# Optimization experiments

Measured on AMD Instinct MI355X. Metric: run time of the kernel, lower is better.

The kernel has to match this reference:

```python
import jax, jax.numpy as jnp
import numpy as np

SOM = (32, 32)   # som_dim; SOM[0]*SOM[1] == num_embeddings
LR = 0.05


def setup_inputs() -> dict:
    key = jax.random.key(0)
    k1, k2 = jax.random.split(key)
    B, K, D = 65536, 1024, 256
    x = jax.random.normal(k1, (B, D), dtype=jnp.float32)
    embeddings = jax.random.uniform(k2, (K, D), dtype=jnp.float32)  # torch.rand init
    return {"x": x, "embeddings": embeddings}


def reference(x, embeddings):
    K, D = embeddings.shape
    # pairwise squared distances: [B, K]
    dist = (jnp.sum(x * x, axis=1, keepdims=True)
            + jnp.sum(embeddings * embeddings, axis=1)
            - 2.0 * (x @ embeddings.T))
    n_min = jnp.argmin(dist, axis=1)          # [B]
    z_q = embeddings[n_min]                   # [B, D]

    # SOM grid coordinates and clamped neighbors
    n_x = n_min // SOM[1]
    n_y = n_min % SOM[1]
    x_up = jnp.where(n_x < SOM[0] - 1, n_x + 1, n_x)
    x_down = jnp.where(n_x > 0, n_x - 1, n_x)
    y_right = jnp.where(n_y < SOM[1] - 1, n_y + 1, n_y)
    y_left = jnp.where(n_y > 0, n_y - 1, n_y)
    idx_up = x_up * SOM[1] + n_y
    idx_down = x_down * SOM[1] + n_y
    idx_right = n_x * SOM[1] + y_right
    idx_left = n_x * SOM[1] + y_left

    # [B, 4, D] neighbor gather (order: up, down, left, right as in torch code)
    nbr_idx = jnp.stack([idx_up, idx_down, idx_left, idx_right], axis=1)
    z_q_neighbors = embeddings[nbr_idx]

    # SOM scatter update (torch does one-hot matmuls; segment_sum is the fused form)
    dw = x - z_q                              # [B, D]
    seg = lambda idx: jax.ops.segment_sum(dw, idx, num_segments=K)
    new_embeddings = jax.lax.stop_gradient(
        embeddings
        + LR * seg(n_min)
        + 0.5 * LR * (seg(idx_up) + seg(idx_down) + seg(idx_right) + seg(idx_left))
    )

    commit_loss = jnp.mean((x - z_q) ** 2)
    som_loss = jnp.mean((jax.lax.stop_gradient(x)[:, None, :] - z_q_neighbors) ** 2)
    return z_q, commit_loss, som_loss, new_embeddings
```

## Files before the change

### kernel.cpp

```cpp
#include <hip/hip_runtime.h>

#define B_ROWS 65536
#define DDIM   256
#define KEMB   1024
#define LRC    0.05f
#define BM 64
#define BN 128

typedef __attribute__((ext_vector_type(8))) _Float16 half8;
typedef __attribute__((ext_vector_type(4))) float f32x4;

#define SX_OFF    0u
#define CNT_OFF   1048576u
#define SUMS_OFF  1052672u
#define ESQ_OFF   1053312u
#define CUR_OFF   1057408u
#define NMIN_OFF  1061504u
#define ROWS_OFF  1585792u
#define EH_OFF    1847936u

static __device__ __forceinline__ unsigned short f2h(float f) {
  _Float16 h = (_Float16)f;
  return *(unsigned short*)&h;
}
static __device__ __forceinline__ float h2f(unsigned short u) {
  _Float16 h = *(_Float16*)&u;
  return (float)h;
}
static __device__ __forceinline__ void glds16(const void* g, void* l) {
  __builtin_amdgcn_global_load_lds(
      (const __attribute__((address_space(1))) unsigned int*)g,
      (__attribute__((address_space(3))) unsigned int*)l, 16, 0, 0);
}

__global__ __launch_bounds__(256) void convert_kernel(
    const float* __restrict__ E, unsigned short* __restrict__ Eh,
    float* __restrict__ esq) {
  size_t i = (size_t)blockIdx.x * 256 + threadIdx.x;
  size_t off = i * 8;
  const float4 v0 = *(const float4*)(E + off);
  const float4 v1 = *(const float4*)(E + off + 4);
  float f[8] = {v0.x, v0.y, v0.z, v0.w, v1.x, v1.y, v1.z, v1.w};
  unsigned short h[8];
  float part = 0.f;
#pragma unroll
  for (int j = 0; j < 8; ++j) {
    h[j] = f2h(f[j]);
    part += f[j] * f[j];
  }
  *(uint4*)(Eh + off) = *(const uint4*)h;
  float s = part;
  for (int o = 16; o > 0; o >>= 1) s += __shfl_down(s, o, 32);
  if ((threadIdx.x & 31) == 0) esq[i >> 5] = s;
}

__global__ __launch_bounds__(256, 2) void gemm_argmin_kernel(
    const float* __restrict__ X, const unsigned short* __restrict__ EhW,
    const float* __restrict__ esq, const float* __restrict__ Ef,
    int* __restrict__ nmin, int* __restrict__ counts, float* __restrict__ zq,
    double* __restrict__ sums) {
  __shared__ __align__(16) unsigned short sX[2][8][256][8];
  __shared__ __align__(16) unsigned short sE[2][512][8];

  const int tid  = threadIdx.x;
  const int lane = tid & 63, w = tid >> 6;
  const int lrow = lane & 15;
  const int qidx = lane >> 4;
  const int rowbase = (w >> 1) * 32;
  const int colb    = (w & 1) * 64;
  const int bm0 = (int)blockIdx.x * BM;

  int ec_row[2], ec_q8[2];
#pragma unroll
  for (int j = 0; j < 2; ++j) {
    const int c = j * 256 + tid;
    ec_row[j] = c >> 2;
    ec_q8[j]  = ((c & 3) ^ ((ec_row[j] >> 1) & 3)) * 8;
  }

#pragma unroll
  for (int j = 0; j < 2; ++j)
    glds16(EhW + (size_t)ec_row[j] * DDIM + ec_q8[j], (char*)&sE[0][j * 256 + tid][0]);

  {
    float part = 0.f;
#pragma unroll
    for (int it = 0; it < 8; ++it) {
      const int c   = it * 256 + tid;
      const int kcc = c >> 8;
      const int cc  = c & 255;
      const int row = cc >> 2;
      const int q   = (cc & 3) ^ ((row >> 1) & 3);
      const float* xp = X + (size_t)(bm0 + row) * DDIM + kcc * 32 + q * 8;
      const float4 a = *(const float4*)xp;
      const float4 b = *(const float4*)(xp + 4);
      float f[8] = {a.x, a.y, a.z, a.w, b.x, b.y, b.z, b.w};
      unsigned short hh[8], ll[8];
#pragma unroll
      for (int m = 0; m < 8; ++m) {
        hh[m] = f2h(f[m]);
        ll[m] = f2h(f[m] - h2f(hh[m]));
        part += f[m] * f[m];
      }
      *(uint4*)((char*)sX + (size_t)c * 16)          = *(const uint4*)hh;
      *(uint4*)((char*)sX + (size_t)(c + 2048) * 16) = *(const uint4*)ll;
    }
#pragma unroll
    for (int o = 32; o > 0; o >>= 1) part += __shfl_down(part, o);
    if (lane == 0)
      atomicAdd(&sums[8 + (((int)blockIdx.x * 4 + w) & 63)], (double)part);
  }

  float rbest[8];
  int   ridx[8];
#pragma unroll
  for (int i = 0; i < 8; ++i) { rbest[i] = 3.4e38f; ridx[i] = 0; }

  int ra[2], rb[4];
#pragma unroll
  for (int t = 0; t < 2; ++t) {
    const int m = rowbase + t * 16 + lrow;
    ra[t] = (m << 2) | (qidx ^ ((m >> 1) & 3));
  }
#pragma unroll
  for (int t = 0; t < 4; ++t) {
    const int n = colb + t * 16 + lrow;
    rb[t] = (n << 2) | (qidx ^ ((n >> 1) & 3));
  }

  __syncthreads();

  for (int nt = 0; nt < 8; ++nt) {
    f32x4 acc[2][4];
#pragma unroll
    for (int i = 0; i < 2; ++i)
#pragma unroll
      for (int j = 0; j < 4; ++j) acc[i][j] = (f32x4){0.f, 0.f, 0.f, 0.f};

#pragma unroll
    for (int kcc = 0; kcc < 8; ++kcc) {
      const int s   = nt * 8 + kcc;
      const int cur = s & 1;
      if (s < 63) {
        const int ns = s + 1;
        const int nnt = ns >> 3, nk = ns & 7;
#pragma unroll
        for (int j = 0; j < 2; ++j) {
          const int c = j * 256 + tid;
          glds16(EhW + (size_t)(nnt * BN + ec_row[j]) * DDIM + nk * 32 + ec_q8[j],
                 (char*)&sE[cur ^ 1][c][0]);
        }
      }
      half8 af0[2], af1[2], bfr[4];
#pragma unroll
      for (int t = 0; t < 2; ++t) {
        af0[t] = *(const half8*)&sX[0][kcc][ra[t]][0];
        af1[t] = *(const half8*)&sX[1][kcc][ra[t]][0];
      }
#pragma unroll
      for (int t = 0; t < 4; ++t) bfr[t] = *(const half8*)&sE[cur][rb[t]][0];
#pragma unroll
      for (int tr = 0; tr < 2; ++tr)
#pragma unroll
        for (int tc = 0; tc < 4; ++tc)
          acc[tr][tc] = __builtin_amdgcn_mfma_f32_16x16x32_f16(
              af0[tr], bfr[tc], acc[tr][tc], 0, 0, 0);
#pragma unroll
      for (int tr = 0; tr < 2; ++tr)
#pragma unroll
        for (int tc = 0; tc < 4; ++tc)
          acc[tr][tc] = __builtin_amdgcn_mfma_f32_16x16x32_f16(
              af1[tr], bfr[tc], acc[tr][tc], 0, 0, 0);
      __syncthreads();
    }
#pragma unroll
    for (int tc = 0; tc < 4; ++tc) {
      const int col = nt * BN + colb + tc * 16 + lrow;
      const float eq = esq[col];
#pragma unroll
      for (int tr = 0; tr < 2; ++tr)
#pragma unroll
        for (int rr = 0; rr < 4; ++rr) {
          float d = eq - 2.0f * acc[tr][tc][rr];
          const int slot = tr * 4 + rr;
          if (d < rbest[slot]) { rbest[slot] = d; ridx[slot] = col; }
        }
    }
  }

  float* cdd = (float*)&sE[0][0][0];
  int*   cdi = (int*)(cdd + 128);
  int*   snm = cdi + 128;
  int*   h   = (int*)&sX[0][0][0][0];

#pragma unroll
  for (int i = 0; i < 4; ++i) h[tid + i * 256] = 0;

#pragma unroll
  for (int slot = 0; slot < 8; ++slot) {
    float bd = rbest[slot];
    int   bi = ridx[slot];
#pragma unroll
    for (int off = 1; off < 16; off <<= 1) {
      float od = __shfl_xor(bd, off, 64);
      int   oi = __shfl_xor(bi, off, 64);
      if (od < bd || (od == bd && oi < bi)) { bd = od; bi = oi; }
    }
    if (lrow == 0) {
      const int row = rowbase + (slot >> 2) * 16 + (lane >> 4) * 4 + (slot & 3);
      cdd[(w & 1) * 64 + row] = bd;
      cdi[(w & 1) * 64 + row] = bi;
    }
  }
  __syncthreads();
  if (tid < BM) {
    float d0 = cdd[tid], d1 = cdd[64 + tid];
    int   i0 = cdi[tid], i1 = cdi[64 + tid];
    int bi = (d1 < d0 || (d1 == d0 && i1 < i0)) ? i1 : i0;
    nmin[bm0 + tid] = bi;
    snm[tid] = bi;
    atomicAdd(&h[bi], 1);
  }
  __syncthreads();
#pragma unroll
  for (int i = 0; i < 4; ++i) {
    int v = h[tid + i * 256];
    if (v) atomicAdd(&counts[tid + i * 256], v);
  }
  const int r0 = w * 16;
#pragma unroll 4
  for (int r = 0; r < 16; ++r) {
    const int k = snm[r0 + r];
    const float4 v = *(const float4*)(Ef + (size_t)k * DDIM + lane * 4);
    *(float4*)(zq + (size_t)(bm0 + r0 + r) * DDIM + lane * 4) = v;
  }
}

__global__ __launch_bounds__(1024) void scan_kernel(
    const int* __restrict__ counts, int* __restrict__ cur) {
  __shared__ int tmp[KEMB];
  int tid = threadIdx.x;
  int v = counts[tid];
  tmp[tid] = v;
  __syncthreads();
  for (int off = 1; off < 1024; off <<= 1) {
    int u = (tid >= off) ? tmp[tid - off] : 0;
    __syncthreads();
    tmp[tid] += u;
    __syncthreads();
  }
  cur[tid] = tmp[tid] - v;
}

__global__ __launch_bounds__(1024) void scatter_kernel(
    const int* __restrict__ nm, int* __restrict__ cur,
    int* __restrict__ rows) {
  __shared__ int lcnt[KEMB], lbase[KEMB], lrank[KEMB];
  int tid = threadIdx.x;
  lcnt[tid] = 0; lrank[tid] = 0;
  __syncthreads();
  int b = blockIdx.x * 1024 + tid;
  int k = nm[b];
  atomicAdd(&lcnt[k], 1);
  __syncthreads();
  if (lcnt[tid] > 0) lbase[tid] = atomicAdd(&cur[tid], lcnt[tid]);
  __syncthreads();
  int r = atomicAdd(&lrank[k], 1);
  rows[lbase[k] + r] = b;
}

__global__ __launch_bounds__(256) void sxsum_kernel(
    const int* __restrict__ rows, const int* __restrict__ nm,
    const float* __restrict__ X, float* __restrict__ SX) {
  __shared__ int sb[32], sk[32];
  int tid = threadIdx.x;
  int p0 = blockIdx.x * 32;
  if (tid < 32) sb[tid] = rows[p0 + tid];
  __syncthreads();
  if (tid < 32) sk[tid] = nm[sb[tid]];
  __syncthreads();
  float acc = 0.f;
  int kprev = sk[0];
  for (int i = 0; i < 32; ++i) {
    int k = sk[i];
    if (k != kprev) {
      atomicAdd(&SX[(size_t)kprev * DDIM + tid], acc);
      acc = 0.f;
      kprev = k;
    }
    acc += X[(size_t)sb[i] * DDIM + tid];
  }
  atomicAdd(&SX[(size_t)kprev * DDIM + tid], acc);
}

__global__ __launch_bounds__(256) void stencil_kernel(
    const float* __restrict__ E, const float* __restrict__ SX,
    const int* __restrict__ counts, const float* __restrict__ esq,
    double* __restrict__ sums, float* __restrict__ out) {
  __shared__ float redc[256], reds[256];
  int k = blockIdx.x, t = threadIdx.x;
  int kx = k >> 5, ky = k & 31;
  int j1 = (kx >= 1)  ? k - 32 : k;
  int j2 = (kx <= 30) ? k + 32 : k;
  int j3 = (ky >= 1)  ? k - 1  : k;
  int j4 = (ky <= 30) ? k + 1  : k;
  int fU = (kx < 31) ? k + 32 : k;
  int fD = (kx > 0)  ? k - 32 : k;
  int fL = (ky > 0)  ? k - 1  : k;
  int fR = (ky < 31) ? k + 1  : k;

  float e   = E[(size_t)k * DDIM + t];
  float sxk = SX[(size_t)k * DDIM + t];
  float Tk = sxk - (float)counts[k] * e;
  float T1 = SX[(size_t)j1 * DDIM + t] - (float)counts[j1] * E[(size_t)j1 * DDIM + t];
  float T2 = SX[(size_t)j2 * DDIM + t] - (float)counts[j2] * E[(size_t)j2 * DDIM + t];
  float T3 = SX[(size_t)j3 * DDIM + t] - (float)counts[j3] * E[(size_t)j3 * DDIM + t];
  float T4 = SX[(size_t)j4 * DDIM + t] - (float)counts[j4] * E[(size_t)j4 * DDIM + t];
  float v = e + LRC * Tk + 0.5f * LRC * (T1 + T2 + T3 + T4);
  out[(size_t)B_ROWS * DDIM + 2 + (size_t)k * DDIM + t] = v;

  float eU = E[(size_t)fU * DDIM + t], eD = E[(size_t)fD * DDIM + t];
  float eL = E[(size_t)fL * DDIM + t], eR = E[(size_t)fR * DDIM + t];
  float cp = -2.f * sxk * e;
  float sp = -2.f * sxk * (eU + eD + eL + eR);
  if (t == 0) {
    float ck = (float)counts[k];
    cp += ck * esq[k];
    sp += ck * (esq[fU] + esq[fD] + esq[fL] + esq[fR]);
  }
  redc[t] = cp; reds[t] = sp;
  __syncthreads();
  for (int s = 128; s > 0; s >>= 1) {
    if (t < s) { redc[t] += redc[t + s]; reds[t] += reds[t + s]; }
    __syncthreads();
  }
  if (t == 0) {
    atomicAdd(&sums[1], (double)redc[0]);
    atomicAdd(&sums[2], (double)reds[0]);
  }
}

__global__ void finalize_kernel(const double* __restrict__ sums,
                                float* __restrict__ out) {
  double xsq = 0.0;
  for (int s = 0; s < 64; ++s) xsq += sums[8 + s];
  out[(size_t)B_ROWS * DDIM]     = (float)((xsq + sums[1]) / ((double)B_ROWS * DDIM));
  out[(size_t)B_ROWS * DDIM + 1] =
      (float)((4.0 * xsq + sums[2]) / ((double)B_ROWS * 4.0 * DDIM));
}

extern "C" void kernel_launch(void* const* d_in, const int* in_sizes, int n_in,
                              void* d_out, int out_size, void* d_ws, size_t ws_size,
                              hipStream_t stream) {
  const float* X = (const float*)d_in[0];
  const float* E = (const float*)d_in[1];
  float* out = (float*)d_out;
  char* ws = (char*)d_ws;

  float*          SX   = (float*)(ws + SX_OFF);
  int*            cnts = (int*)(ws + CNT_OFF);
  double*         sums = (double*)(ws + SUMS_OFF);
  float*          esq  = (float*)(ws + ESQ_OFF);
  int*            cur  = (int*)(ws + CUR_OFF);
  int*            nm   = (int*)(ws + NMIN_OFF);
  int*            rows = (int*)(ws + ROWS_OFF);
  unsigned short* EhW  = (unsigned short*)(ws + EH_OFF);

  hipMemsetAsync(ws, 0, ESQ_OFF, stream);

  convert_kernel<<<KEMB * (DDIM / 8) / 256, 256, 0, stream>>>(E, EhW, esq);
  gemm_argmin_kernel<<<B_ROWS / BM, 256, 0, stream>>>(X, EhW, esq, E, nm, cnts, out,
                                                      sums);
  scan_kernel<<<1, 1024, 0, stream>>>(cnts, cur);
  scatter_kernel<<<B_ROWS / 1024, 1024, 0, stream>>>(nm, cur, rows);
  sxsum_kernel<<<B_ROWS / 32, 256, 0, stream>>>(rows, nm, X, SX);
  stencil_kernel<<<KEMB, 256, 0, stream>>>(E, SX, cnts, esq, sums, out);
  finalize_kernel<<<1, 1, 0, stream>>>(sums, out);
}
```

Measured before the change: 250.3 us.

## Hoist X fragments to registers and restructure scatter and segment-sum kernels

The GEMM-argmin kernel now loads all A-operand (X) fragments from LDS into registers once, before the N-tile loop, instead of reloading them for each of the 8 column tiles. The scatter kernel moves to 256-thread blocks that each handle 1024 codebook slots with a 4-way loop. The segment-sum kernel gives each block 64 sorted rows, has each thread load 16 rows as float4 and accumulate 4 lanes at once, so it issues fewer atomics per element. The register hoist costs 32 extra half8 registers per thread, which may lower occupancy or cause spills. Smaller scatter blocks raise the number of global atomics on the cursors.

```diff
diff --git a/kernel.cpp b/kernel.cpp
--- a/kernel.cpp
+++ b/kernel.cpp
@@ -130,6 +130,15 @@
 
   __syncthreads();
 
+  half8 a0[8][2], a1[8][2];
+#pragma unroll
+  for (int kcc = 0; kcc < 8; ++kcc)
+#pragma unroll
+    for (int t = 0; t < 2; ++t) {
+      a0[kcc][t] = *(const half8*)&sX[0][kcc][ra[t]][0];
+      a1[kcc][t] = *(const half8*)&sX[1][kcc][ra[t]][0];
+    }
+
   for (int nt = 0; nt < 8; ++nt) {
     f32x4 acc[2][4];
 #pragma unroll
@@ -151,12 +160,7 @@
                  (char*)&sE[cur ^ 1][c][0]);
         }
       }
-      half8 af0[2], af1[2], bfr[4];
-#pragma unroll
-      for (int t = 0; t < 2; ++t) {
-        af0[t] = *(const half8*)&sX[0][kcc][ra[t]][0];
-        af1[t] = *(const half8*)&sX[1][kcc][ra[t]][0];
-      }
+      half8 bfr[4];
 #pragma unroll
       for (int t = 0; t < 4; ++t) bfr[t] = *(const half8*)&sE[cur][rb[t]][0];
 #pragma unroll
@@ -164,13 +168,13 @@
 #pragma unroll
         for (int tc = 0; tc < 4; ++tc)
           acc[tr][tc] = __builtin_amdgcn_mfma_f32_16x16x32_f16(
-              af0[tr], bfr[tc], acc[tr][tc], 0, 0, 0);
+              a0[kcc][tr], bfr[tc], acc[tr][tc], 0, 0, 0);
 #pragma unroll
       for (int tr = 0; tr < 2; ++tr)
 #pragma unroll
         for (int tc = 0; tc < 4; ++tc)
           acc[tr][tc] = __builtin_amdgcn_mfma_f32_16x16x32_f16(
-              af1[tr], bfr[tc], acc[tr][tc], 0, 0, 0);
+              a1[kcc][tr], bfr[tc], acc[tr][tc], 0, 0, 0);
       __syncthreads();
     }
 #pragma unroll
@@ -252,18 +256,23 @@
   cur[tid] = tmp[tid] - v;
 }
 
-__global__ __launch_bounds__(1024) void scatter_kernel(
+__global__ __launch_bounds__(256) void scatter_kernel(
     const int* __restrict__ nm, int* __restrict__ cur,
     int* __restrict__ rows) {
   __shared__ int lcnt[KEMB], lbase[KEMB], lrank[KEMB];
   int tid = threadIdx.x;
-  lcnt[tid] = 0; lrank[tid] = 0;
-  __syncthreads();
-  int b = blockIdx.x * 1024 + tid;
+#pragma unroll
+  for (int i = 0; i < 4; ++i) { lcnt[tid + i * 256] = 0; lrank[tid + i * 256] = 0; }
+  __syncthreads();
+  int b = blockIdx.x * 256 + tid;
   int k = nm[b];
   atomicAdd(&lcnt[k], 1);
   __syncthreads();
-  if (lcnt[tid] > 0) lbase[tid] = atomicAdd(&cur[tid], lcnt[tid]);
+#pragma unroll
+  for (int i = 0; i < 4; ++i) {
+    int kk = tid + i * 256;
+    if (lcnt[kk] > 0) lbase[kk] = atomicAdd(&cur[kk], lcnt[kk]);
+  }
   __syncthreads();
   int r = atomicAdd(&lrank[k], 1);
   rows[lbase[k] + r] = b;
@@ -272,25 +281,36 @@
 __global__ __launch_bounds__(256) void sxsum_kernel(
     const int* __restrict__ rows, const int* __restrict__ nm,
     const float* __restrict__ X, float* __restrict__ SX) {
-  __shared__ int sb[32], sk[32];
+  __shared__ int sb[64], sk[64];
   int tid = threadIdx.x;
-  int p0 = blockIdx.x * 32;
-  if (tid < 32) sb[tid] = rows[p0 + tid];
-  __syncthreads();
-  if (tid < 32) sk[tid] = nm[sb[tid]];
-  __syncthreads();
-  float acc = 0.f;
-  int kprev = sk[0];
-  for (int i = 0; i < 32; ++i) {
-    int k = sk[i];
+  int p0 = blockIdx.x * 64;
+  if (tid < 64) sb[tid] = rows[p0 + tid];
+  __syncthreads();
+  if (tid < 64) sk[tid] = nm[sb[tid]];
+  __syncthreads();
+  const int g = tid >> 6;
+  const int l = tid & 63;
+  float4 xv[16];
+#pragma unroll
+  for (int i = 0; i < 16; ++i)
+    xv[i] = *(const float4*)(X + (size_t)sb[g * 16 + i] * DDIM + l * 4);
+  float ax = 0.f, ay = 0.f, az = 0.f, aw = 0.f;
+  int kprev = sk[g * 16];
+#pragma unroll
+  for (int i = 0; i < 16; ++i) {
+    int k = sk[g * 16 + i];
     if (k != kprev) {
-      atomicAdd(&SX[(size_t)kprev * DDIM + tid], acc);
-      acc = 0.f;
+      float* p = SX + (size_t)kprev * DDIM + l * 4;
+      atomicAdd(p + 0, ax); atomicAdd(p + 1, ay);
+      atomicAdd(p + 2, az); atomicAdd(p + 3, aw);
+      ax = ay = az = aw = 0.f;
       kprev = k;
     }
-    acc += X[(size_t)sb[i] * DDIM + tid];
-  }
-  atomicAdd(&SX[(size_t)kprev * DDIM + tid], acc);
+    ax += xv[i].x; ay += xv[i].y; az += xv[i].z; aw += xv[i].w;
+  }
+  float* p = SX + (size_t)kprev * DDIM + l * 4;
+  atomicAdd(p + 0, ax); atomicAdd(p + 1, ay);
+  atomicAdd(p + 2, az); atomicAdd(p + 3, aw);
 }
 
 __global__ __launch_bounds__(256) void stencil_kernel(
@@ -372,8 +392,8 @@
   gemm_argmin_kernel<<<B_ROWS / BM, 256, 0, stream>>>(X, EhW, esq, E, nm, cnts, out,
                                                       sums);
   scan_kernel<<<1, 1024, 0, stream>>>(cnts, cur);
-  scatter_kernel<<<B_ROWS / 1024, 1024, 0, stream>>>(nm, cur, rows);
-  sxsum_kernel<<<B_ROWS / 32, 256, 0, stream>>>(rows, nm, X, SX);
+  scatter_kernel<<<B_ROWS / 256, 256, 0, stream>>>(nm, cur, rows);
+  sxsum_kernel<<<B_ROWS / 64, 256, 0, stream>>>(rows, nm, X, SX);
   stencil_kernel<<<KEMB, 256, 0, stream>>>(E, SX, cnts, esq, sums, out);
   finalize_kernel<<<1, 1, 0, stream>>>(sums, out);
 }
```

New measurement: 270.1 us. 1.08x slower.

## Hoist A fragments to registers and fold scan and finalize kernels into neighbors

Applied to the files above, without the earlier changes.

The GEMM-argmin kernel now loads all X fragments from shared memory into registers once, before the N-tile loop, instead of reloading them in every iteration. The separate prefix-scan kernel is merged into the scatter kernel: each block recomputes the scan redundantly and adds it to an atomic cursor that is now zeroed by the memset. The finalize kernel is replaced by a last-block-done counter in the stencil kernel. These changes remove two launches and repeated LDS reads, at the cost of higher register pressure (32 extra half8 values, which may lower occupancy) and redundant scan work in every scatter block.

```diff
diff --git a/kernel.cpp b/kernel.cpp
--- a/kernel.cpp
+++ b/kernel.cpp
@@ -130,6 +130,15 @@
 
   __syncthreads();
 
+  half8 a0[8][2], a1[8][2];
+#pragma unroll
+  for (int kcc = 0; kcc < 8; ++kcc)
+#pragma unroll
+    for (int t = 0; t < 2; ++t) {
+      a0[kcc][t] = *(const half8*)&sX[0][kcc][ra[t]][0];
+      a1[kcc][t] = *(const half8*)&sX[1][kcc][ra[t]][0];
+    }
+
   for (int nt = 0; nt < 8; ++nt) {
     f32x4 acc[2][4];
 #pragma unroll
@@ -151,12 +160,7 @@
                  (char*)&sE[cur ^ 1][c][0]);
         }
       }
-      half8 af0[2], af1[2], bfr[4];
-#pragma unroll
-      for (int t = 0; t < 2; ++t) {
-        af0[t] = *(const half8*)&sX[0][kcc][ra[t]][0];
-        af1[t] = *(const half8*)&sX[1][kcc][ra[t]][0];
-      }
+      half8 bfr[4];
 #pragma unroll
       for (int t = 0; t < 4; ++t) bfr[t] = *(const half8*)&sE[cur][rb[t]][0];
 #pragma unroll
@@ -164,13 +168,13 @@
 #pragma unroll
         for (int tc = 0; tc < 4; ++tc)
           acc[tr][tc] = __builtin_amdgcn_mfma_f32_16x16x32_f16(
-              af0[tr], bfr[tc], acc[tr][tc], 0, 0, 0);
+              a0[kcc][tr], bfr[tc], acc[tr][tc], 0, 0, 0);
 #pragma unroll
       for (int tr = 0; tr < 2; ++tr)
 #pragma unroll
         for (int tc = 0; tc < 4; ++tc)
           acc[tr][tc] = __builtin_amdgcn_mfma_f32_16x16x32_f16(
-              af1[tr], bfr[tc], acc[tr][tc], 0, 0, 0);
+              a1[kcc][tr], bfr[tc], acc[tr][tc], 0, 0, 0);
       __syncthreads();
     }
 #pragma unroll
@@ -236,34 +240,27 @@
   }
 }
 
-__global__ __launch_bounds__(1024) void scan_kernel(
-    const int* __restrict__ counts, int* __restrict__ cur) {
-  __shared__ int tmp[KEMB];
-  int tid = threadIdx.x;
-  int v = counts[tid];
-  tmp[tid] = v;
-  __syncthreads();
-  for (int off = 1; off < 1024; off <<= 1) {
-    int u = (tid >= off) ? tmp[tid - off] : 0;
-    __syncthreads();
-    tmp[tid] += u;
-    __syncthreads();
-  }
-  cur[tid] = tmp[tid] - v;
-}
-
 __global__ __launch_bounds__(1024) void scatter_kernel(
-    const int* __restrict__ nm, int* __restrict__ cur,
-    int* __restrict__ rows) {
-  __shared__ int lcnt[KEMB], lbase[KEMB], lrank[KEMB];
+    const int* __restrict__ counts, const int* __restrict__ nm,
+    int* __restrict__ cur, int* __restrict__ rows) {
+  __shared__ int lcnt[KEMB], lbase[KEMB], lrank[KEMB], scn[KEMB];
   int tid = threadIdx.x;
   lcnt[tid] = 0; lrank[tid] = 0;
-  __syncthreads();
+  int v = counts[tid];
+  scn[tid] = v;
+  __syncthreads();
+  for (int off = 1; off < 1024; off <<= 1) {
+    int u = (tid >= off) ? scn[tid - off] : 0;
+    __syncthreads();
+    scn[tid] += u;
+    __syncthreads();
+  }
   int b = blockIdx.x * 1024 + tid;
   int k = nm[b];
   atomicAdd(&lcnt[k], 1);
   __syncthreads();
-  if (lcnt[tid] > 0) lbase[tid] = atomicAdd(&cur[tid], lcnt[tid]);
+  if (lcnt[tid] > 0)
+    lbase[tid] = (scn[tid] - v) + atomicAdd(&cur[tid], lcnt[tid]);
   __syncthreads();
   int r = atomicAdd(&lrank[k], 1);
   rows[lbase[k] + r] = b;
@@ -337,16 +334,19 @@
   if (t == 0) {
     atomicAdd(&sums[1], (double)redc[0]);
     atomicAdd(&sums[2], (double)reds[0]);
-  }
-}
-
-__global__ void finalize_kernel(const double* __restrict__ sums,
-                                float* __restrict__ out) {
-  double xsq = 0.0;
-  for (int s = 0; s < 64; ++s) xsq += sums[8 + s];
-  out[(size_t)B_ROWS * DDIM]     = (float)((xsq + sums[1]) / ((double)B_ROWS * DDIM));
-  out[(size_t)B_ROWS * DDIM + 1] =
-      (float)((4.0 * xsq + sums[2]) / ((double)B_ROWS * 4.0 * DDIM));
+    __threadfence();
+    unsigned int prev = atomicAdd((unsigned int*)&sums[0], 1u);
+    if (prev == KEMB - 1) {
+      volatile const double* vs = (volatile const double*)sums;
+      double xsq = 0.0;
+#pragma unroll
+      for (int s2 = 0; s2 < 64; ++s2) xsq += vs[8 + s2];
+      double c1 = vs[1], c2 = vs[2];
+      out[(size_t)B_ROWS * DDIM]     = (float)((xsq + c1) / ((double)B_ROWS * DDIM));
+      out[(size_t)B_ROWS * DDIM + 1] =
+          (float)((4.0 * xsq + c2) / ((double)B_ROWS * 4.0 * DDIM));
+    }
+  }
 }
 
 extern "C" void kernel_launch(void* const* d_in, const int* in_sizes, int n_in,
@@ -366,14 +366,12 @@
   int*            rows = (int*)(ws + ROWS_OFF);
   unsigned short* EhW  = (unsigned short*)(ws + EH_OFF);
 
-  hipMemsetAsync(ws, 0, ESQ_OFF, stream);
+  hipMemsetAsync(ws, 0, NMIN_OFF, stream);
 
   convert_kernel<<<KEMB * (DDIM / 8) / 256, 256, 0, stream>>>(E, EhW, esq);
   gemm_argmin_kernel<<<B_ROWS / BM, 256, 0, stream>>>(X, EhW, esq, E, nm, cnts, out,
                                                       sums);
-  scan_kernel<<<1, 1024, 0, stream>>>(cnts, cur);
-  scatter_kernel<<<B_ROWS / 1024, 1024, 0, stream>>>(nm, cur, rows);
+  scatter_kernel<<<B_ROWS / 1024, 1024, 0, stream>>>(cnts, nm, cur, rows);
   sxsum_kernel<<<B_ROWS / 32, 256, 0, stream>>>(rows, nm, X, SX);
   stencil_kernel<<<KEMB, 256, 0, stream>>>(E, SX, cnts, esq, sums, out);
-  finalize_kernel<<<1, 1, 0, stream>>>(sums, out);
-}
+}
```

Result: slower. 259.4 us (+3.6%).
